# Kernel optimization log

Hardware: AMD Instinct MI355X
Metric: run time of the kernel (lower is better)

## Reference

```python
import jax, jax.numpy as jnp
import numpy as np

B, C, N = 64, 512, 512  # batch, channels (=in_dim), last dim (=in_dim)
OUT = 512
GROUPS = 32
EPS = 1e-5


def setup_inputs() -> dict:
    key = jax.random.key(0)
    ks = jax.random.split(key, 7)
    s = 1.0 / np.sqrt(C)
    return {
        "x": jax.random.normal(ks[0], (B, C, N), dtype=jnp.float32),
        "q_w": jax.random.normal(ks[1], (OUT, C), dtype=jnp.float32) * s,
        "q_b": jax.random.normal(ks[2], (OUT,), dtype=jnp.float32) * s,
        "k_w": jax.random.normal(ks[3], (OUT, C), dtype=jnp.float32) * s,
        "k_b": jax.random.normal(ks[4], (OUT,), dtype=jnp.float32) * s,
        "v_w": jax.random.normal(ks[5], (OUT, C), dtype=jnp.float32) * s,
        "v_b": jax.random.normal(ks[6], (OUT,), dtype=jnp.float32) * s,
        "gn_w": jnp.ones((C,), dtype=jnp.float32),
        "gn_b": jnp.zeros((C,), dtype=jnp.float32),
    }


def group_norm(x, w, b):
    # x: (B, C, N); 32 groups over channel dim, affine per-channel.
    Bb, Cc, Nn = x.shape
    xg = x.reshape(Bb, GROUPS, -1)
    mean = jnp.mean(xg, axis=-1, keepdims=True)
    var = jnp.var(xg, axis=-1, keepdims=True)
    xn = ((xg - mean) * jax.lax.rsqrt(var + EPS)).reshape(Bb, Cc, Nn)
    return xn * w[None, :, None] + b[None, :, None]


def reference(x, q_w, q_b, k_w, k_b, v_w, v_b, gn_w, gn_b):
    xn = group_norm(x, gn_w, gn_b)  # (B, C, N)
    # nn.Linear applies to the last dim (N == in_dim)
    q = jnp.einsum("bcn,dn->bcd", xn, q_w) + q_b  # (B, C, OUT)
    k = jnp.einsum("bcn,dn->bcd", xn, k_w) + k_b
    v = jnp.einsum("bcn,dn->bcd", xn, v_w) + v_b
    scale = 1.0 / jnp.sqrt(jnp.float32(OUT))
    scores = jnp.einsum("bqd,bkd->bqk", q, k) * scale  # (B, C, C)
    attn = jax.nn.softmax(scores, axis=-1)
    return jnp.einsum("bqk,bkd->bqd", attn, v)  # (B, C, OUT)
```

## Files before the change

### kernel.cpp

```cpp
#include <hip/hip_runtime.h>
#include <cstdint>

#define EPSV 1e-5f
#define SM_SCALE 0.044194173824159216f

typedef unsigned short u16;
typedef __attribute__((ext_vector_type(8))) short short8;
typedef __attribute__((ext_vector_type(4))) float f32x4;

__device__ __forceinline__ u16 f2bf(float f) {
  union { float f; uint32_t u; } v; v.f = f;
  return (u16)((v.u + 0x7FFFu + ((v.u >> 16) & 1u)) >> 16);
}

__device__ __forceinline__ void gload_lds16(const void* g, void* l) {
  __builtin_amdgcn_global_load_lds((const __attribute__((address_space(1))) void*)g,
                                   (__attribute__((address_space(3))) void*)l, 16, 0, 0);
}

__device__ __forceinline__ f32x4 mfma16(short8 a, short8 b, f32x4 c) {
  return __builtin_amdgcn_mfma_f32_16x16x32_bf16(a, b, c, 0, 0, 0);
}

__device__ __forceinline__ const short8* lds_frag(const u16* t, int row, int cc) {
  return reinterpret_cast<const short8*>(t + (size_t)(((row << 2) + (cc ^ ((row >> 1) & 3))) << 3));
}

#define WAIT_ENTER(N, is_tail)                                      \
  if (is_tail) { asm volatile("s_waitcnt vmcnt(0)" ::: "memory"); } \
  else         { asm volatile("s_waitcnt vmcnt(" #N ")" ::: "memory"); } \
  __builtin_amdgcn_s_barrier();                                     \
  asm volatile("" ::: "memory");

#define WAIT_EXIT()                                                 \
  asm volatile("s_waitcnt lgkmcnt(0)" ::: "memory");                \
  __builtin_amdgcn_s_barrier();                                     \
  asm volatile("" ::: "memory");

__global__ __launch_bounds__(256) void gn_fused_k(const float* __restrict__ x,
                                                  const float* __restrict__ gw,
                                                  const float* __restrict__ gb,
                                                  u16* __restrict__ xn) {
  __shared__ float xs[8192];
  __shared__ float ls[4], lss[4];
  const int bg = blockIdx.x;
  const int g = bg & 31;
  const float* p = x + (size_t)bg * 8192;
  float s = 0.f, ss = 0.f;
#pragma unroll
  for (int i = 0; i < 8; ++i) {
    const int idx = i * 1024 + threadIdx.x * 4;
    float4 v = *reinterpret_cast<const float4*>(p + idx);
    *reinterpret_cast<float4*>(xs + idx) = v;
    s += v.x + v.y + v.z + v.w;
    ss += v.x * v.x + v.y * v.y + v.z * v.z + v.w * v.w;
  }
  for (int off = 32; off; off >>= 1) { s += __shfl_xor(s, off); ss += __shfl_xor(ss, off); }
  const int w = threadIdx.x >> 6;
  if ((threadIdx.x & 63) == 0) { ls[w] = s; lss[w] = ss; }
  __syncthreads();
  s = ls[0] + ls[1] + ls[2] + ls[3];
  ss = lss[0] + lss[1] + lss[2] + lss[3];
  const float inv_n = 1.0f / 8192.f;
  const float mean = s * inv_n;
  const float rstd = rsqrtf(ss * inv_n - mean * mean + EPSV);
#pragma unroll
  for (int j = 0; j < 4; ++j) {
    const int idx = j * 2048 + threadIdx.x * 8;
    const int c = g * 16 + (idx >> 9);
    const float sc = gw[c] * rstd;
    const float sh = gb[c] - mean * sc;
    u16 o[8];
#pragma unroll
    for (int e = 0; e < 8; ++e) o[e] = f2bf(xs[idx + e] * sc + sh);
    *reinterpret_cast<uint4*>(xn + (size_t)bg * 8192 + idx) = *reinterpret_cast<const uint4*>(o);
  }
}

__global__ __launch_bounds__(256) void cast3_k(const float* __restrict__ a,
                                               const float* __restrict__ b2,
                                               const float* __restrict__ c,
                                               u16* __restrict__ oa, u16* __restrict__ ob,
                                               u16* __restrict__ oc) {
  const int which = blockIdx.x >> 7;
  const float* in = which == 0 ? a : (which == 1 ? b2 : c);
  u16* out = which == 0 ? oa : (which == 1 ? ob : oc);
  size_t base = (((size_t)(blockIdx.x & 127)) * 256 + threadIdx.x) * 8;
  float4 v0 = *reinterpret_cast<const float4*>(in + base);
  float4 v1 = *reinterpret_cast<const float4*>(in + base + 4);
  u16 o[8];
  o[0] = f2bf(v0.x); o[1] = f2bf(v0.y); o[2] = f2bf(v0.z); o[3] = f2bf(v0.w);
  o[4] = f2bf(v1.x); o[5] = f2bf(v1.y); o[6] = f2bf(v1.z); o[7] = f2bf(v1.w);
  *reinterpret_cast<uint4*>(out + base) = *reinterpret_cast<const uint4*>(o);
}

template <int OUT_MODE>
__global__ __launch_bounds__(256, 3) void gemm_abt_k(const u16* __restrict__ A, size_t sA,
                                                     const u16* __restrict__ Bm, size_t sB,
                                                     const float* __restrict__ bias,
                                                     void* __restrict__ out, size_t sO) {
  __shared__ u16 As[2][4096];
  __shared__ u16 Bs[2][4096];
  const int d = blockIdx.x;
  const int t = d >> 3;
  const int b = (d & 7) * 8 + (t >> 4);
  const int tile = t & 15;
  const int tm = (tile >> 2) * 128, tn = (tile & 3) * 128;
  const u16* Ab = A + (size_t)b * sA;
  const u16* Bb = Bm + (size_t)b * sB;
  const int tid = threadIdx.x, w = tid >> 6, lane = tid & 63;
  const int wr = (w >> 1) * 64, wc = (w & 1) * 64;
  const int srow = lane >> 2;
  const int ssw = ((lane & 3) ^ ((lane >> 3) & 3)) * 8;
  f32x4 acc[4][4] = {};

#define GM_STAGE(bb, k0)                                                       \
  {                                                                            \
    _Pragma("unroll")                                                          \
    for (int s2 = 0; s2 < 4; ++s2) {                                           \
      const int c = w * 4 + s2;                                                \
      if (c < 8)                                                               \
        gload_lds16(Ab + (size_t)(tm + c * 16 + srow) * 512 + (k0) + ssw,      \
                    &As[bb][c * 512]);                                         \
      else                                                                     \
        gload_lds16(Bb + (size_t)(tn + (c - 8) * 16 + srow) * 512 + (k0) + ssw,\
                    &Bs[bb][(c - 8) * 512]);                                   \
    }                                                                          \
  }

  GM_STAGE(0, 0);
  GM_STAGE(1, 32);
  for (int ts = 0; ts < 16; ++ts) {
    const int cur = ts & 1;
    WAIT_ENTER(4, ts == 15);
    const int frow = lane & 15, cc = lane >> 4;
    short8 af[4], bf[4];
#pragma unroll
    for (int i = 0; i < 4; ++i) {
      af[i] = *lds_frag(As[cur], wr + i * 16 + frow, cc);
      bf[i] = *lds_frag(Bs[cur], wc + i * 16 + frow, cc);
    }
#pragma unroll
    for (int mi = 0; mi < 4; ++mi)
#pragma unroll
      for (int ni = 0; ni < 4; ++ni)
        acc[mi][ni] = mfma16(af[mi], bf[ni], acc[mi][ni]);
    WAIT_EXIT();
    if (ts < 14) GM_STAGE(cur, (ts + 2) * 32);
  }
#undef GM_STAGE

  const int col0 = lane & 15, row0 = (lane >> 4) * 4;
#pragma unroll
  for (int mi = 0; mi < 4; ++mi)
#pragma unroll
    for (int ni = 0; ni < 4; ++ni) {
      const int gc = tn + wc + ni * 16 + col0;
      const float bv = (OUT_MODE == 0) ? bias[gc] : 0.f;
#pragma unroll
      for (int r = 0; r < 4; ++r) {
        const int gr = tm + wr + mi * 16 + row0 + r;
        float v = acc[mi][ni][r];
        if (OUT_MODE == 0) v += bv;
        if (OUT_MODE == 1) v += bias[gr];
        if (OUT_MODE == 2)
          ((float*)out)[(size_t)b * sO + (size_t)gr * 512 + gc] = v;
        else
          ((u16*)out)[(size_t)b * sO + (size_t)gr * 512 + gc] = f2bf(v);
      }
    }
}

__global__ __launch_bounds__(256, 2) void scores_softmax_k(const u16* __restrict__ Q,
                                                           const u16* __restrict__ K,
                                                           u16* __restrict__ P) {
  __shared__ u16 Qs[2][2048];
  __shared__ u16 Ks[2][16384];
  __shared__ float rmax[4][64], rsum[4][64];
  const int d = blockIdx.x;
  const int t = d >> 3;
  const int b = (d & 7) * 8 + (t >> 3);
  const int m0 = (t & 7) * 64;
  const u16* Qb = Q + (size_t)b * 262144 + (size_t)m0 * 512;
  const u16* Kb = K + (size_t)b * 262144;
  u16* Pb = P + (size_t)b * 262144;
  const int tid = threadIdx.x, kq = tid >> 6, lane = tid & 63;
  const int srow = lane >> 2;
  const int ssw = ((lane & 3) ^ ((lane >> 3) & 3)) * 8;
  f32x4 acc[4][8] = {};

#define SC_STAGE(bb, k0)                                                       \
  {                                                                            \
    _Pragma("unroll")                                                          \
    for (int s2 = 0; s2 < 8; ++s2) {                                           \
      const int c = kq * 8 + s2;                                               \
      gload_lds16(Kb + (size_t)(c * 16 + srow) * 512 + (k0) + ssw,             \
                  &Ks[bb][c * 512]);                                           \
    }                                                                          \
    gload_lds16(Qb + (size_t)(kq * 16 + srow) * 512 + (k0) + ssw,              \
                &Qs[bb][kq * 512]);                                            \
  }

  SC_STAGE(0, 0);
  SC_STAGE(1, 32);
  for (int ts = 0; ts < 16; ++ts) {
    const int cur = ts & 1;
    WAIT_ENTER(9, ts == 15);
    const int frow = lane & 15, cc = lane >> 4;
    short8 aq[4];
#pragma unroll
    for (int i = 0; i < 4; ++i)
      aq[i] = *lds_frag(Qs[cur], i * 16 + frow, cc);
#pragma unroll
    for (int j = 0; j < 8; ++j) {
      short8 bk = *lds_frag(Ks[cur], kq * 128 + j * 16 + frow, cc);
#pragma unroll
      for (int i = 0; i < 4; ++i)
        acc[i][j] = mfma16(aq[i], bk, acc[i][j]);
    }
    WAIT_EXIT();
    if (ts < 14) SC_STAGE(cur, (ts + 2) * 32);
  }
#undef SC_STAGE

  float pm[4][4];
#pragma unroll
  for (int i = 0; i < 4; ++i)
#pragma unroll
    for (int r = 0; r < 4; ++r) pm[i][r] = -1e30f;
#pragma unroll
  for (int i = 0; i < 4; ++i)
#pragma unroll
    for (int j = 0; j < 8; ++j)
#pragma unroll
      for (int r = 0; r < 4; ++r) {
        float v = acc[i][j][r] * SM_SCALE;
        acc[i][j][r] = v;
        pm[i][r] = fmaxf(pm[i][r], v);
      }
#pragma unroll
  for (int off = 1; off < 16; off <<= 1)
#pragma unroll
    for (int i = 0; i < 4; ++i)
#pragma unroll
      for (int r = 0; r < 4; ++r) pm[i][r] = fmaxf(pm[i][r], __shfl_xor(pm[i][r], off));
  if ((lane & 15) == 0) {
#pragma unroll
    for (int i = 0; i < 4; ++i)
#pragma unroll
      for (int r = 0; r < 4; ++r)
        rmax[kq][i * 16 + (lane >> 4) * 4 + r] = pm[i][r];
  }
  __syncthreads();
#pragma unroll
  for (int i = 0; i < 4; ++i)
#pragma unroll
    for (int r = 0; r < 4; ++r) {
      const int row = i * 16 + (lane >> 4) * 4 + r;
      pm[i][r] = fmaxf(fmaxf(rmax[0][row], rmax[1][row]), fmaxf(rmax[2][row], rmax[3][row]));
    }
  float ps[4][4];
#pragma unroll
  for (int i = 0; i < 4; ++i)
#pragma unroll
    for (int r = 0; r < 4; ++r) ps[i][r] = 0.f;
#pragma unroll
  for (int i = 0; i < 4; ++i)
#pragma unroll
    for (int j = 0; j < 8; ++j)
#pragma unroll
      for (int r = 0; r < 4; ++r) {
        float e = __expf(acc[i][j][r] - pm[i][r]);
        acc[i][j][r] = e;
        ps[i][r] += e;
      }
#pragma unroll
  for (int off = 1; off < 16; off <<= 1)
#pragma unroll
    for (int i = 0; i < 4; ++i)
#pragma unroll
      for (int r = 0; r < 4; ++r) ps[i][r] += __shfl_xor(ps[i][r], off);
  if ((lane & 15) == 0) {
#pragma unroll
    for (int i = 0; i < 4; ++i)
#pragma unroll
      for (int r = 0; r < 4; ++r)
        rsum[kq][i * 16 + (lane >> 4) * 4 + r] = ps[i][r];
  }
  __syncthreads();
#pragma unroll
  for (int i = 0; i < 4; ++i)
#pragma unroll
    for (int r = 0; r < 4; ++r) {
      const int row = i * 16 + (lane >> 4) * 4 + r;
      ps[i][r] = 1.0f / (rsum[0][row] + rsum[1][row] + rsum[2][row] + rsum[3][row]);
    }
#pragma unroll
  for (int i = 0; i < 4; ++i)
#pragma unroll
    for (int j = 0; j < 8; ++j) {
      const int gcol = kq * 128 + j * 16 + (lane & 15);
#pragma unroll
      for (int r = 0; r < 4; ++r) {
        const int grow = m0 + i * 16 + (lane >> 4) * 4 + r;
        Pb[(size_t)grow * 512 + gcol] = f2bf(acc[i][j][r] * ps[i][r]);
      }
    }
}

extern "C" void kernel_launch(void* const* d_in, const int* in_sizes, int n_in,
                              void* d_out, int out_size, void* d_ws, size_t ws_size,
                              hipStream_t stream) {
  const float* x = (const float*)d_in[0];
  const float* qw = (const float*)d_in[1];
  const float* qb = (const float*)d_in[2];
  const float* kw = (const float*)d_in[3];
  const float* kb = (const float*)d_in[4];
  const float* vw = (const float*)d_in[5];
  const float* vb = (const float*)d_in[6];
  const float* gnw = (const float*)d_in[7];
  const float* gnb = (const float*)d_in[8];

  char* ws = (char*)d_ws;
  u16* qwb = (u16*)(ws);
  u16* kwb = (u16*)(ws + 524288);
  u16* vwb = (u16*)(ws + 2 * 524288);
  u16* xn = (u16*)(ws + 4 * 524288);
  u16* Qb = xn + 16777216;
  u16* Kb = Qb + 16777216;
  u16* VT = Kb + 16777216;
  u16* P = xn;
  float* out = (float*)d_out;

  gn_fused_k<<<dim3(2048), dim3(256), 0, stream>>>(x, gnw, gnb, xn);
  cast3_k<<<dim3(384), dim3(256), 0, stream>>>(qw, kw, vw, qwb, kwb, vwb);
  gemm_abt_k<0><<<dim3(1024), dim3(256), 0, stream>>>(xn, (size_t)262144, qwb, (size_t)0, qb, (void*)Qb, (size_t)262144);
  gemm_abt_k<0><<<dim3(1024), dim3(256), 0, stream>>>(xn, (size_t)262144, kwb, (size_t)0, kb, (void*)Kb, (size_t)262144);
  gemm_abt_k<1><<<dim3(1024), dim3(256), 0, stream>>>(vwb, (size_t)0, xn, (size_t)262144, vb, (void*)VT, (size_t)262144);
  scores_softmax_k<<<dim3(512), dim3(256), 0, stream>>>(Qb, Kb, P);
  gemm_abt_k<2><<<dim3(1024), dim3(256), 0, stream>>>(P, (size_t)262144, VT, (size_t)262144, (const float*)nullptr, (void*)out, (size_t)262144);
}
```

Before: 168.3 us.

## Fuse scores-softmax with PV matmul, keeping probabilities in shared memory

The softmax probability tile is written to a swizzled LDS buffer that reuses the K staging space, and the block then multiplies it by V^T directly, streaming V^T fragments from global memory into registers with double buffering. This removes the bf16 P round trip through global memory and one kernel launch. In exchange each block does twice the MFMA work with a single 64-row tile per block (512 blocks), reads V^T from global memory without LDS staging, and holds more registers. The GEMM launch bound also changes from 3 to 2 blocks per CU.

Result: no change. 170.3 us (+1.2%).

```diff
diff --git a/kernel.cpp b/kernel.cpp
--- a/kernel.cpp
+++ b/kernel.cpp
@@ -95,10 +95,10 @@
 }
 
 template <int OUT_MODE>
-__global__ __launch_bounds__(256, 3) void gemm_abt_k(const u16* __restrict__ A, size_t sA,
+__global__ __launch_bounds__(256, 2) void gemm_abt_k(const u16* __restrict__ A, size_t sA,
                                                      const u16* __restrict__ Bm, size_t sB,
                                                      const float* __restrict__ bias,
-                                                     void* __restrict__ out, size_t sO) {
+                                                     u16* __restrict__ out, size_t sO) {
   __shared__ u16 As[2][4096];
   __shared__ u16 Bs[2][4096];
   const int d = blockIdx.x;
@@ -163,19 +163,16 @@
         float v = acc[mi][ni][r];
         if (OUT_MODE == 0) v += bv;
         if (OUT_MODE == 1) v += bias[gr];
-        if (OUT_MODE == 2)
-          ((float*)out)[(size_t)b * sO + (size_t)gr * 512 + gc] = v;
-        else
-          ((u16*)out)[(size_t)b * sO + (size_t)gr * 512 + gc] = f2bf(v);
-      }
-    }
-}
-
-__global__ __launch_bounds__(256, 2) void scores_softmax_k(const u16* __restrict__ Q,
-                                                           const u16* __restrict__ K,
-                                                           u16* __restrict__ P) {
-  __shared__ u16 Qs[2][2048];
-  __shared__ u16 Ks[2][16384];
+        out[(size_t)b * sO + (size_t)gr * 512 + gc] = f2bf(v);
+      }
+    }
+}
+
+__global__ __launch_bounds__(256, 2) void attn_fused_k(const u16* __restrict__ Q,
+                                                       const u16* __restrict__ K,
+                                                       const u16* __restrict__ VT,
+                                                       float* __restrict__ out) {
+  __shared__ u16 smem[36864];
   __shared__ float rmax[4][64], rsum[4][64];
   const int d = blockIdx.x;
   const int t = d >> 3;
@@ -183,10 +180,14 @@
   const int m0 = (t & 7) * 64;
   const u16* Qb = Q + (size_t)b * 262144 + (size_t)m0 * 512;
   const u16* Kb = K + (size_t)b * 262144;
-  u16* Pb = P + (size_t)b * 262144;
+  const u16* VTb = VT + (size_t)b * 262144;
   const int tid = threadIdx.x, kq = tid >> 6, lane = tid & 63;
   const int srow = lane >> 2;
   const int ssw = ((lane & 3) ^ ((lane >> 3) & 3)) * 8;
+  const int frow = lane & 15, cc = lane >> 4;
+  u16* Ks0 = smem;
+  u16* Qs0 = smem + 32768;
+  u16* Psm = smem;
   f32x4 acc[4][8] = {};
 
 #define SC_STAGE(bb, k0)                                                       \
@@ -195,10 +196,10 @@
     for (int s2 = 0; s2 < 8; ++s2) {                                           \
       const int c = kq * 8 + s2;                                               \
       gload_lds16(Kb + (size_t)(c * 16 + srow) * 512 + (k0) + ssw,             \
-                  &Ks[bb][c * 512]);                                           \
+                  Ks0 + (bb) * 16384 + c * 512);                               \
     }                                                                          \
     gload_lds16(Qb + (size_t)(kq * 16 + srow) * 512 + (k0) + ssw,              \
-                &Qs[bb][kq * 512]);                                            \
+                Qs0 + (bb) * 2048 + kq * 512);                                 \
   }
 
   SC_STAGE(0, 0);
@@ -206,14 +207,13 @@
   for (int ts = 0; ts < 16; ++ts) {
     const int cur = ts & 1;
     WAIT_ENTER(9, ts == 15);
-    const int frow = lane & 15, cc = lane >> 4;
     short8 aq[4];
 #pragma unroll
     for (int i = 0; i < 4; ++i)
-      aq[i] = *lds_frag(Qs[cur], i * 16 + frow, cc);
+      aq[i] = *lds_frag(Qs0 + cur * 2048, i * 16 + frow, cc);
 #pragma unroll
     for (int j = 0; j < 8; ++j) {
-      short8 bk = *lds_frag(Ks[cur], kq * 128 + j * 16 + frow, cc);
+      short8 bk = *lds_frag(Ks0 + cur * 16384, kq * 128 + j * 16 + frow, cc);
 #pragma unroll
       for (int i = 0; i < 4; ++i)
         acc[i][j] = mfma16(aq[i], bk, acc[i][j]);
@@ -295,6 +295,64 @@
       const int row = i * 16 + (lane >> 4) * 4 + r;
       ps[i][r] = 1.0f / (rsum[0][row] + rsum[1][row] + rsum[2][row] + rsum[3][row]);
     }
+
+  const u16* VTw = VTb + (size_t)(kq * 128 + frow) * 512 + cc * 8;
+  short8 vA[8], vB[8];
+#define VTLOAD(vr, k0)                                                         \
+  {                                                                            \
+    _Pragma("unroll")                                                          \
+    for (int j = 0; j < 8; ++j)                                                \
+      vr[j] = *reinterpret_cast<const short8*>(VTw + (size_t)j * 8192 + (k0)); \
+  }
+  VTLOAD(vA, 0);
+  VTLOAD(vB, 32);
+
+#pragma unroll
+  for (int i = 0; i < 4; ++i)
+#pragma unroll
+    for (int j = 0; j < 8; ++j) {
+      const int col = kq * 128 + j * 16 + (lane & 15);
+#pragma unroll
+      for (int r = 0; r < 4; ++r) {
+        const int row = i * 16 + (lane >> 4) * 4 + r;
+        Psm[row * 512 + (((col >> 3) ^ (row & 7)) << 3) + (col & 7)] =
+            f2bf(acc[i][j][r] * ps[i][r]);
+      }
+    }
+  __syncthreads();
+
+#pragma unroll
+  for (int i = 0; i < 4; ++i)
+#pragma unroll
+    for (int j = 0; j < 8; ++j) acc[i][j] = (f32x4){0.f, 0.f, 0.f, 0.f};
+
+#define PV_BODY(vr, ts)                                                        \
+  {                                                                            \
+    short8 pa[4];                                                              \
+    _Pragma("unroll")                                                          \
+    for (int i = 0; i < 4; ++i) {                                              \
+      const int prow = i * 16 + frow;                                          \
+      const int slot = (ts) * 4 + cc;                                          \
+      pa[i] = *reinterpret_cast<const short8*>(                                \
+          &Psm[prow * 512 + ((slot ^ (prow & 7)) << 3)]);                      \
+    }                                                                          \
+    _Pragma("unroll")                                                          \
+    for (int j = 0; j < 8; ++j)                                                \
+      _Pragma("unroll")                                                        \
+      for (int i = 0; i < 4; ++i)                                              \
+        acc[i][j] = mfma16(pa[i], vr[j], acc[i][j]);                           \
+    if ((ts) < 14) VTLOAD(vr, ((ts) + 2) * 32);                                \
+  }
+
+#pragma unroll
+  for (int t2 = 0; t2 < 8; ++t2) {
+    PV_BODY(vA, t2 * 2);
+    PV_BODY(vB, t2 * 2 + 1);
+  }
+#undef PV_BODY
+#undef VTLOAD
+
+  float* ob = out + (size_t)b * 262144;
 #pragma unroll
   for (int i = 0; i < 4; ++i)
 #pragma unroll
@@ -303,7 +361,7 @@
 #pragma unroll
       for (int r = 0; r < 4; ++r) {
         const int grow = m0 + i * 16 + (lane >> 4) * 4 + r;
-        Pb[(size_t)grow * 512 + gcol] = f2bf(acc[i][j][r] * ps[i][r]);
+        ob[(size_t)grow * 512 + gcol] = acc[i][j][r];
       }
     }
 }
@@ -329,14 +387,12 @@
   u16* Qb = xn + 16777216;
   u16* Kb = Qb + 16777216;
   u16* VT = Kb + 16777216;
-  u16* P = xn;
   float* out = (float*)d_out;
 
   gn_fused_k<<<dim3(2048), dim3(256), 0, stream>>>(x, gnw, gnb, xn);
   cast3_k<<<dim3(384), dim3(256), 0, stream>>>(qw, kw, vw, qwb, kwb, vwb);
-  gemm_abt_k<0><<<dim3(1024), dim3(256), 0, stream>>>(xn, (size_t)262144, qwb, (size_t)0, qb, (void*)Qb, (size_t)262144);
-  gemm_abt_k<0><<<dim3(1024), dim3(256), 0, stream>>>(xn, (size_t)262144, kwb, (size_t)0, kb, (void*)Kb, (size_t)262144);
-  gemm_abt_k<1><<<dim3(1024), dim3(256), 0, stream>>>(vwb, (size_t)0, xn, (size_t)262144, vb, (void*)VT, (size_t)262144);
-  scores_softmax_k<<<dim3(512), dim3(256), 0, stream>>>(Qb, Kb, P);
-  gemm_abt_k<2><<<dim3(1024), dim3(256), 0, stream>>>(P, (size_t)262144, VT, (size_t)262144, (const float*)nullptr, (void*)out, (size_t)262144);
-}
+  gemm_abt_k<0><<<dim3(1024), dim3(256), 0, stream>>>(xn, (size_t)262144, qwb, (size_t)0, qb, Qb, (size_t)262144);
+  gemm_abt_k<0><<<dim3(1024), dim3(256), 0, stream>>>(xn, (size_t)262144, kwb, (size_t)0, kb, Kb, (size_t)262144);
+  gemm_abt_k<1><<<dim3(1024), dim3(256), 0, stream>>>(vwb, (size_t)0, xn, (size_t)262144, vb, VT, (size_t)262144);
+  attn_fused_k<<<dim3(512), dim3(256), 0, stream>>>(Qb, Kb, VT, out);
+}
```

## Replace 128x128 GEMM with 256x256 tiled 8-wave kernel and phased prefetch

Applied to the files above, without the earlier changes.

Replaces the 128x128-tile batched GEMM (256 threads, 3 blocks/CU) with a 256x256-tile kernel using 512 threads, 128KB LDS, and a multi-phase software pipeline. Loads are staged in 64-wide K half-tiles with XOR swizzling, interleaved with MFMA phases using vmcnt waits, barriers and s_setprio. This is meant to raise arithmetic intensity and hide load latency. The cost is only 256 workgroups on 256 CUs (one wave of blocks), higher register pressure, and occupancy of one block per CU.

Result: faster. 148.1 us (-12.0%).

```diff
diff --git a/kernel.cpp b/kernel.cpp
--- a/kernel.cpp
+++ b/kernel.cpp
@@ -95,72 +95,121 @@
 }
 
 template <int OUT_MODE>
-__global__ __launch_bounds__(256, 3) void gemm_abt_k(const u16* __restrict__ A, size_t sA,
-                                                     const u16* __restrict__ Bm, size_t sB,
-                                                     const float* __restrict__ bias,
-                                                     void* __restrict__ out, size_t sO) {
-  __shared__ u16 As[2][4096];
-  __shared__ u16 Bs[2][4096];
+__global__ __launch_bounds__(512, 1) void gemm256_k(const u16* __restrict__ A, size_t sA,
+                                                    const u16* __restrict__ Bm, size_t sB,
+                                                    const float* __restrict__ bias,
+                                                    void* __restrict__ out, size_t sO) {
+  __shared__ u16 smem[65536];
   const int d = blockIdx.x;
-  const int t = d >> 3;
-  const int b = (d & 7) * 8 + (t >> 4);
-  const int tile = t & 15;
-  const int tm = (tile >> 2) * 128, tn = (tile & 3) * 128;
+  const int wgid = (d & 7) * 32 + (d >> 3);
+  const int b = wgid >> 2;
+  const int tile = wgid & 3;
+  const int tm = (tile >> 1) * 256, tn = (tile & 1) * 256;
   const u16* Ab = A + (size_t)b * sA;
   const u16* Bb = Bm + (size_t)b * sB;
   const int tid = threadIdx.x, w = tid >> 6, lane = tid & 63;
-  const int wr = (w >> 1) * 64, wc = (w & 1) * 64;
-  const int srow = lane >> 2;
-  const int ssw = ((lane & 3) ^ ((lane >> 3) & 3)) * 8;
-  f32x4 acc[4][4] = {};
-
-#define GM_STAGE(bb, k0)                                                       \
+  const int rh = w >> 2, cw = w & 3;
+  const int frow = lane & 15, cc = lane >> 4;
+  f32x4 acc[8][4] = {};
+  short8 af[8], bfr[2];
+
+#define STAGEH(Lofs, Gp)                                                       \
   {                                                                            \
+    const u16* gsrc_ = (Gp);                                                   \
     _Pragma("unroll")                                                          \
-    for (int s2 = 0; s2 < 4; ++s2) {                                           \
-      const int c = w * 4 + s2;                                                \
-      if (c < 8)                                                               \
-        gload_lds16(Ab + (size_t)(tm + c * 16 + srow) * 512 + (k0) + ssw,      \
-                    &As[bb][c * 512]);                                         \
-      else                                                                     \
-        gload_lds16(Bb + (size_t)(tn + (c - 8) * 16 + srow) * 512 + (k0) + ssw,\
-                    &Bs[bb][(c - 8) * 512]);                                   \
-    }                                                                          \
-  }
-
-  GM_STAGE(0, 0);
-  GM_STAGE(1, 32);
-  for (int ts = 0; ts < 16; ++ts) {
-    const int cur = ts & 1;
-    WAIT_ENTER(4, ts == 15);
-    const int frow = lane & 15, cc = lane >> 4;
-    short8 af[4], bf[4];
-#pragma unroll
-    for (int i = 0; i < 4; ++i) {
-      af[i] = *lds_frag(As[cur], wr + i * 16 + frow, cc);
-      bf[i] = *lds_frag(Bs[cur], wc + i * 16 + frow, cc);
-    }
-#pragma unroll
-    for (int mi = 0; mi < 4; ++mi)
-#pragma unroll
-      for (int ni = 0; ni < 4; ++ni)
-        acc[mi][ni] = mfma16(af[mi], bf[ni], acc[mi][ni]);
-    WAIT_EXIT();
-    if (ts < 14) GM_STAGE(cur, (ts + 2) * 32);
-  }
-#undef GM_STAGE
+    for (int p_ = 0; p_ < 2; ++p_) {                                           \
+      const int row_ = p_ * 64 + (tid >> 3);                                   \
+      const int slot_ = (tid & 7) ^ (row_ & 7);                                \
+      gload_lds16(gsrc_ + (size_t)row_ * 512 + slot_ * 8,                      \
+                  &smem[(Lofs) + p_ * 4096 + tid * 8]);                        \
+    }                                                                          \
+  }
+
+#define PHASE(VMN, QB, KS, CP, ...)                                            \
+  {                                                                            \
+    asm volatile("s_waitcnt vmcnt(" #VMN ")" ::: "memory");                    \
+    __builtin_amdgcn_s_barrier();                                              \
+    asm volatile("" ::: "memory");                                             \
+    _Pragma("unroll")                                                          \
+    for (int j_ = 0; j_ < 2; ++j_) {                                           \
+      const int lrb_ = (cw & 1) * 64 + (CP) * 32 + j_ * 16 + frow;             \
+      bfr[j_] = *reinterpret_cast<const short8*>(                              \
+          &smem[(QB) + 16384 + (cw >> 1) * 8192 + lrb_ * 64 +                  \
+                (((KS) * 4 + cc) ^ (lrb_ & 7)) * 8]);                          \
+    }                                                                          \
+    if ((CP) == 0) {                                                           \
+      _Pragma("unroll")                                                        \
+      for (int ri_ = 0; ri_ < 8; ++ri_) {                                      \
+        const int lra_ = ri_ * 16 + frow;                                      \
+        af[ri_] = *reinterpret_cast<const short8*>(                            \
+            &smem[(QB) + rh * 8192 + lra_ * 64 +                               \
+                  (((KS) * 4 + cc) ^ (lra_ & 7)) * 8]);                        \
+      }                                                                        \
+    }                                                                          \
+    __VA_ARGS__                                                                \
+    __builtin_amdgcn_s_setprio(1);                                             \
+    _Pragma("unroll")                                                          \
+    for (int ri_ = 0; ri_ < 8; ++ri_) {                                        \
+      acc[ri_][(CP) * 2]     = mfma16(af[ri_], bfr[0], acc[ri_][(CP) * 2]);    \
+      acc[ri_][(CP) * 2 + 1] = mfma16(af[ri_], bfr[1], acc[ri_][(CP) * 2 + 1]);\
+    }                                                                          \
+    __builtin_amdgcn_s_setprio(0);                                             \
+    __builtin_amdgcn_s_barrier();                                              \
+    asm volatile("" ::: "memory");                                             \
+  }
+
+  STAGEH(0,     Ab + (size_t)tm * 512);
+  STAGEH(8192,  Ab + (size_t)(tm + 128) * 512);
+  STAGEH(16384, Bb + (size_t)tn * 512);
+  STAGEH(24576, Bb + (size_t)(tn + 128) * 512);
+  STAGEH(32768, Ab + (size_t)tm * 512 + 64);
+
+  for (int i = 0; i < 3; ++i) {
+    const int k0c1 = i * 128 + 64;
+    const int k0n2 = i * 128 + 128;
+    const int k0n3 = i * 128 + 192;
+    PHASE(2, 0, 0, 0,
+          STAGEH(40960, Ab + (size_t)(tm + 128) * 512 + k0c1);
+          STAGEH(49152, Bb + (size_t)tn * 512 + k0c1);)
+    PHASE(6, 0, 0, 1,
+          STAGEH(57344, Bb + (size_t)(tn + 128) * 512 + k0c1);)
+    PHASE(6, 0, 1, 0, )
+    PHASE(2, 0, 1, 1,
+          STAGEH(0, Ab + (size_t)tm * 512 + k0n2);)
+    PHASE(2, 32768, 0, 0,
+          STAGEH(8192,  Ab + (size_t)(tm + 128) * 512 + k0n2);
+          STAGEH(16384, Bb + (size_t)tn * 512 + k0n2);)
+    PHASE(6, 32768, 0, 1,
+          STAGEH(24576, Bb + (size_t)(tn + 128) * 512 + k0n2);)
+    PHASE(6, 32768, 1, 0, )
+    PHASE(2, 32768, 1, 1,
+          STAGEH(32768, Ab + (size_t)tm * 512 + k0n3);)
+  }
+  PHASE(2, 0, 0, 0,
+        STAGEH(40960, Ab + (size_t)(tm + 128) * 512 + 448);
+        STAGEH(49152, Bb + (size_t)tn * 512 + 448);)
+  PHASE(6, 0, 0, 1,
+        STAGEH(57344, Bb + (size_t)(tn + 128) * 512 + 448);)
+  PHASE(6, 0, 1, 0, )
+  PHASE(2, 0, 1, 1, )
+  PHASE(0, 32768, 0, 0, )
+  PHASE(0, 32768, 0, 1, )
+  PHASE(0, 32768, 1, 0, )
+  PHASE(0, 32768, 1, 1, )
+#undef PHASE
+#undef STAGEH
 
   const int col0 = lane & 15, row0 = (lane >> 4) * 4;
 #pragma unroll
-  for (int mi = 0; mi < 4; ++mi)
-#pragma unroll
-    for (int ni = 0; ni < 4; ++ni) {
-      const int gc = tn + wc + ni * 16 + col0;
+  for (int ri = 0; ri < 8; ++ri) {
+#pragma unroll
+    for (int cj = 0; cj < 4; ++cj) {
+      const int gc = tn + cw * 64 + cj * 16 + col0;
       const float bv = (OUT_MODE == 0) ? bias[gc] : 0.f;
 #pragma unroll
       for (int r = 0; r < 4; ++r) {
-        const int gr = tm + wr + mi * 16 + row0 + r;
-        float v = acc[mi][ni][r];
+        const int gr = tm + rh * 128 + ri * 16 + row0 + r;
+        float v = acc[ri][cj][r];
         if (OUT_MODE == 0) v += bv;
         if (OUT_MODE == 1) v += bias[gr];
         if (OUT_MODE == 2)
@@ -169,6 +218,7 @@
           ((u16*)out)[(size_t)b * sO + (size_t)gr * 512 + gc] = f2bf(v);
       }
     }
+  }
 }
 
 __global__ __launch_bounds__(256, 2) void scores_softmax_k(const u16* __restrict__ Q,
@@ -334,9 +384,9 @@
 
   gn_fused_k<<<dim3(2048), dim3(256), 0, stream>>>(x, gnw, gnb, xn);
   cast3_k<<<dim3(384), dim3(256), 0, stream>>>(qw, kw, vw, qwb, kwb, vwb);
-  gemm_abt_k<0><<<dim3(1024), dim3(256), 0, stream>>>(xn, (size_t)262144, qwb, (size_t)0, qb, (void*)Qb, (size_t)262144);
-  gemm_abt_k<0><<<dim3(1024), dim3(256), 0, stream>>>(xn, (size_t)262144, kwb, (size_t)0, kb, (void*)Kb, (size_t)262144);
-  gemm_abt_k<1><<<dim3(1024), dim3(256), 0, stream>>>(vwb, (size_t)0, xn, (size_t)262144, vb, (void*)VT, (size_t)262144);
+  gemm256_k<0><<<dim3(256), dim3(512), 0, stream>>>(xn, (size_t)262144, qwb, (size_t)0, qb, (void*)Qb, (size_t)262144);
+  gemm256_k<0><<<dim3(256), dim3(512), 0, stream>>>(xn, (size_t)262144, kwb, (size_t)0, kb, (void*)Kb, (size_t)262144);
+  gemm256_k<1><<<dim3(256), dim3(512), 0, stream>>>(vwb, (size_t)0, xn, (size_t)262144, vb, (void*)VT, (size_t)262144);
   scores_softmax_k<<<dim3(512), dim3(256), 0, stream>>>(Qb, Kb, P);
-  gemm_abt_k<2><<<dim3(1024), dim3(256), 0, stream>>>(P, (size_t)262144, VT, (size_t)262144, (const float*)nullptr, (void*)out, (size_t)262144);
-}
+  gemm256_k<2><<<dim3(256), dim3(512), 0, stream>>>(P, (size_t)262144, VT, (size_t)262144, (const float*)nullptr, (void*)out, (size_t)262144);
+}
```
